# Kernel optimization log

Hardware: AMD Instinct MI355X
Metric: run time of the kernel (lower is better)

## Reference

```python
import jax, jax.numpy as jnp
from jax import lax
import numpy as np

B, C, H, W = 4, 256, 64, 64
CQK = C // 8  # 32


def conv3x3(x, w, b):
    # x: [B,C_in,H,W], w: [C_out,C_in,3,3], b: [C_out]
    y = lax.conv_general_dilated(x, w, window_strides=(1, 1), padding='SAME',
                                 dimension_numbers=('NCHW', 'OIHW', 'NCHW'))
    return y + b[None, :, None, None]


def setup_inputs() -> dict:
    key = jax.random.key(0)
    ks = jax.random.split(key, 8)
    scale = 0.02
    return {
        'x': jax.random.normal(ks[0], (B, C, H, W), dtype=jnp.float32),
        'wq': jax.random.normal(ks[1], (CQK, C, 3, 3), dtype=jnp.float32) * scale,
        'bq': jax.random.normal(ks[2], (CQK,), dtype=jnp.float32) * scale,
        'wk': jax.random.normal(ks[3], (CQK, C, 3, 3), dtype=jnp.float32) * scale,
        'bk': jax.random.normal(ks[4], (CQK,), dtype=jnp.float32) * scale,
        'wv': jax.random.normal(ks[5], (C, C, 3, 3), dtype=jnp.float32) * scale,
        'bv': jax.random.normal(ks[6], (C,), dtype=jnp.float32) * scale,
        'gamma': jax.random.normal(ks[7], (1,), dtype=jnp.float32) * scale,
    }


def reference(x, wq, bq, wk, bk, wv, bv, gamma):
    b, c, h, w = x.shape
    n = h * w
    # Q: [B, N, C//8]  (permute(0,2,1) of the flattened conv output)
    q = conv3x3(x, wq, bq).reshape(b, -1, n).transpose(0, 2, 1)
    # K: [B, C//8, N]
    k = conv3x3(x, wk, bk).reshape(b, -1, n)
    # s: [B, N_q, N_k]
    s = jnp.einsum('bqd,bdk->bqk', q, k)
    # NOTE: original uses Softmax(dim=-2), i.e. over the QUERY axis
    attn_T = jax.nn.softmax(s, axis=-2)
    # V: [B, C, N]
    v = conv3x3(x, wv, bv).reshape(b, c, n)
    # o = bmm(V, attn_T): [B, C, N]
    o = jnp.einsum('bcq,bqk->bck', v, attn_T).reshape(b, c, h, w)
    return x + gamma * o
```

## Files before the change

### kernel.cpp

```cpp
#include <hip/hip_runtime.h>
#include <cstddef>

#define N_PIX 4096
#define HW 64
#define LOG2E 1.4426950408889634f
#define SHIFT2 28.8539008177793f

typedef __attribute__((ext_vector_type(8))) short bf16x8;
typedef __attribute__((ext_vector_type(4))) float f32x4;

static __device__ __forceinline__ unsigned short f2bf(float f) {
    union { float f; unsigned u; } v; v.f = f;
    unsigned r = v.u + 0x7fffu + ((v.u >> 16) & 1u);
    return (unsigned short)(r >> 16);
}
static __device__ __forceinline__ float bf2f(unsigned short s) {
    union { unsigned u; float f; } v; v.u = (unsigned)s << 16;
    return v.f;
}
static __device__ __forceinline__ unsigned pack_bf16_trunc(float lo, float hi) {
    union { float f; unsigned u; } a, b; a.f = hi; b.f = lo;
    return __builtin_amdgcn_perm(a.u, b.u, 0x07060302u);
}

__global__ __launch_bounds__(256) void x_transpose(
    const float* __restrict__ x, unsigned short* __restrict__ xbf)
{
    __shared__ unsigned short Ts[64][72];
    const int tid = threadIdx.x;
    const int px0 = blockIdx.x * 64, ci0 = blockIdx.y * 64, b = blockIdx.z;
    const float* xb = x + ((size_t)b * 256 + ci0) * N_PIX;

#pragma unroll
    for (int r = 0; r < 4; ++r) {
        int c = r * 16 + (tid >> 4);
        int p4 = (tid & 15) * 4;
        float4 v = *(const float4*)&xb[(size_t)c * N_PIX + px0 + p4];
        Ts[c][p4 + 0] = f2bf(v.x);
        Ts[c][p4 + 1] = f2bf(v.y);
        Ts[c][p4 + 2] = f2bf(v.z);
        Ts[c][p4 + 3] = f2bf(v.w);
    }
    __syncthreads();
#pragma unroll
    for (int r = 0; r < 2; ++r) {
        int id = tid * 2 + r;
        int p = id >> 3, c8 = (id & 7) * 8;
        ushort4 lo, hi;
        lo.x = Ts[c8 + 0][p]; lo.y = Ts[c8 + 1][p];
        lo.z = Ts[c8 + 2][p]; lo.w = Ts[c8 + 3][p];
        hi.x = Ts[c8 + 4][p]; hi.y = Ts[c8 + 5][p];
        hi.z = Ts[c8 + 6][p]; hi.w = Ts[c8 + 7][p];
        size_t off = ((size_t)b * N_PIX + px0 + p) * 256 + ci0 + c8;
        *(ushort4*)&xbf[off]     = lo;
        *(ushort4*)&xbf[off + 4] = hi;
    }
}

__global__ __launch_bounds__(256) void w_transform(
    const float* __restrict__ wq, const float* __restrict__ wk,
    const float* __restrict__ wv, unsigned short* __restrict__ wAll)
{
    int gid = blockIdx.x * 256 + threadIdx.x;
    if (gid >= 72 * 320 * 4) return;
    int part = gid & 3;
    int m = (gid >> 2) % 320;
    int kb = gid / 1280;
    int t = kb >> 3;
    int ci0 = (kb & 7) * 32 + part * 8;
    const float* src; int co; float sc = 1.f;
    if (m < 256)      { src = wv; co = m; }
    else if (m < 288) { src = wq; co = m - 256; sc = LOG2E; }
    else              { src = wk; co = m - 288; }
    ushort4 lo, hi;
    lo.x = f2bf(sc * src[((size_t)co * 256 + ci0 + 0) * 9 + t]);
    lo.y = f2bf(sc * src[((size_t)co * 256 + ci0 + 1) * 9 + t]);
    lo.z = f2bf(sc * src[((size_t)co * 256 + ci0 + 2) * 9 + t]);
    lo.w = f2bf(sc * src[((size_t)co * 256 + ci0 + 3) * 9 + t]);
    hi.x = f2bf(sc * src[((size_t)co * 256 + ci0 + 4) * 9 + t]);
    hi.y = f2bf(sc * src[((size_t)co * 256 + ci0 + 5) * 9 + t]);
    hi.z = f2bf(sc * src[((size_t)co * 256 + ci0 + 6) * 9 + t]);
    hi.w = f2bf(sc * src[((size_t)co * 256 + ci0 + 7) * 9 + t]);
    size_t off = ((size_t)kb * 320 + m) * 32 + part * 8;
    *(ushort4*)&wAll[off]     = lo;
    *(ushort4*)&wAll[off + 4] = hi;
}

__global__ __launch_bounds__(256) void conv_gemm_v2(
    const unsigned short* __restrict__ xbf, const unsigned short* __restrict__ wAll,
    const float* __restrict__ bq, const float* __restrict__ bk,
    const float* __restrict__ bv,
    unsigned short* __restrict__ vbf, unsigned short* __restrict__ qt,
    unsigned short* __restrict__ kt)
{
    const int tid = threadIdx.x;
    const int w = tid >> 6, lane = tid & 63, quad = lane >> 4, l15 = lane & 15;
    const int px0 = blockIdx.x * 128;
    const int mt  = blockIdx.y;
    const int b   = blockIdx.z;
    const bool qk = (mt == 2);
    const int row0 = qk ? 256 : mt * 128;
    const int NCB  = qk ? 2 : 4;
    const int wc0  = (w & 1) * (qk ? 32 : 64);
    const int wp0  = (w >> 1) * 64;

    __shared__ unsigned short Bl[2][128 * 40];

    const unsigned short* xb = xbf + (size_t)b * N_PIX * 256;

    const int brow = tid >> 1;
    const int bp0  = (tid & 1) * 2;
    const int bswz = (brow >> 2) & 3;
    const int py = (px0 + brow) >> 6, pxc = brow & 63;

    f32x4 acc[4][4];
#pragma unroll
    for (int cb = 0; cb < 4; ++cb)
#pragma unroll
        for (int jb = 0; jb < 4; ++jb) acc[cb][jb] = (f32x4){0.f, 0.f, 0.f, 0.f};

    const unsigned short* aBase = wAll + ((size_t)(row0 + wc0 + l15) * 32 + quad * 8);

    auto load_a = [&](int kb, bf16x8* af) {
        const unsigned short* p = aBase + (size_t)kb * (320 * 32);
#pragma unroll
        for (int cb = 0; cb < 4; ++cb)
            if (cb < NCB) af[cb] = *(const bf16x8*)&p[cb * 512];
    };

    bf16x8 bS[2];
    auto load_b = [&](int kb) {
        int t = kb >> 3, ci0 = (kb & 7) << 5;
        int dy = t / 3 - 1, dx = t - (t / 3) * 3 - 1;
        int gy = py + dy, gx = pxc + dx;
        if ((unsigned)gy < 64u && (unsigned)gx < 64u) {
            const unsigned short* s = xb + ((size_t)(gy * 64 + gx) * 256 + ci0 + bp0 * 8);
            bS[0] = *(const bf16x8*)&s[0];
            bS[1] = *(const bf16x8*)&s[8];
        } else {
            bS[0] = (bf16x8){0,0,0,0,0,0,0,0};
            bS[1] = (bf16x8){0,0,0,0,0,0,0,0};
        }
    };
    auto store_b = [&](int buf) {
        int p0 = (bp0 + bswz) & 3;
        int p1 = (bp0 + 1 + bswz) & 3;
        *(bf16x8*)&Bl[buf][brow * 40 + p0 * 8] = bS[0];
        *(bf16x8*)&Bl[buf][brow * 40 + p1 * 8] = bS[1];
    };

    bf16x8 afC[4], afN[4];
    load_a(0, afC);
    load_b(0);
    store_b(0);

    for (int kb = 0; kb < 72; ++kb) {
        __syncthreads();
        const bool hasN = (kb + 1 < 72);
        if (hasN) { load_b(kb + 1); load_a(kb + 1, afN); }

        bf16x8 bf[4];
#pragma unroll
        for (int jb = 0; jb < 4; ++jb) {
            int row = wp0 + jb * 16 + l15;
            int pp = (quad + (row >> 2)) & 3;
            bf[jb] = *(const bf16x8*)&Bl[kb & 1][row * 40 + pp * 8];
        }
#pragma unroll
        for (int cb = 0; cb < 4; ++cb)
            if (cb < NCB)
#pragma unroll
                for (int jb = 0; jb < 4; ++jb)
                    acc[cb][jb] = __builtin_amdgcn_mfma_f32_16x16x32_bf16(
                        afC[cb], bf[jb], acc[cb][jb], 0, 0, 0);

        if (hasN) {
            store_b((kb + 1) & 1);
#pragma unroll
            for (int cb = 0; cb < 4; ++cb) afC[cb] = afN[cb];
        }
    }

    if (!qk) {
#pragma unroll
        for (int cb = 0; cb < 4; ++cb) {
            int c = mt * 128 + wc0 + cb * 16 + quad * 4;
#pragma unroll
            for (int r = 0; r < 4; ++r) {
                float bias = bv[c + r];
#pragma unroll
                for (int jb = 0; jb < 4; ++jb) {
                    int px = px0 + wp0 + jb * 16 + l15;
                    vbf[((size_t)b * 256 + c + r) * N_PIX + px] = f2bf(acc[cb][jb][r] + bias);
                }
            }
        }
    } else {
#pragma unroll
        for (int cb = 0; cb < 2; ++cb) {
            int cl = wc0 + cb * 16 + quad * 4;
#pragma unroll
            for (int r = 0; r < 4; ++r) {
                int c = cl + r;
                float bias = (c < 32) ? bq[c] * LOG2E : bk[c - 32];
#pragma unroll
                for (int jb = 0; jb < 4; ++jb) {
                    int px = px0 + wp0 + jb * 16 + l15;
                    unsigned short val = f2bf(acc[cb][jb][r] + bias);
                    if (c < 32)
                        qt[((size_t)b * N_PIX + px) * 32 + c] = val;
                    else
                        kt[((size_t)b * N_PIX + px) * 32 + (c - 32)] = val;
                }
            }
        }
    }
}

__global__ __launch_bounds__(256, 2) void fused_attn_mfma(
    const unsigned short* __restrict__ qt, const unsigned short* __restrict__ kt,
    const unsigned short* __restrict__ vbf,
    unsigned short* __restrict__ Abuf, float* __restrict__ lbuf, int iRange)
{
    const int tid  = threadIdx.x;
    const int w    = tid >> 6;
    const int lane = tid & 63;
    const int quad = lane >> 4;
    const int l15  = lane & 15;
    const int j0   = blockIdx.x * 128;
    const int b    = blockIdx.y;
    const int sp   = blockIdx.z;
    const int iBeg = sp * iRange;
    const int NI   = iRange / 64;

    const unsigned short* qtb = qt + (size_t)b * N_PIX * 32;
    const unsigned short* ktb = kt + (size_t)b * N_PIX * 32;
    const unsigned short* vb  = vbf + (size_t)b * 256 * N_PIX;

    __shared__ unsigned Pfrag[2][4096];
    __shared__ float lred[4][128];

    bf16x8 kf[8];
#pragma unroll
    for (int jb = 0; jb < 8; ++jb)
        kf[jb] = *(const bf16x8*)&ktb[((size_t)(j0 + jb * 16 + l15)) * 32 + quad * 8];

    f32x4 acc[4][8];
#pragma unroll
    for (int cb = 0; cb < 4; ++cb)
#pragma unroll
        for (int jb = 0; jb < 8; ++jb)
            acc[cb][jb] = (f32x4){0.f, 0.f, 0.f, 0.f};

    float lpart[8] = {0.f, 0.f, 0.f, 0.f, 0.f, 0.f, 0.f, 0.f};

    const int wFrag = w >> 1;
    const int wL    = ((w & 1) << 5) + ((quad >> 1) << 4) + l15;
    const int wEl2  = (quad & 1) << 1;

    bf16x8 va[2][4];

    auto s_phase = [&](bf16x8 qa, int buf) {
#pragma unroll
        for (int jb = 0; jb < 8; ++jb) {
            f32x4 s = __builtin_amdgcn_mfma_f32_16x16x32_bf16(
                qa, kf[jb], (f32x4){-SHIFT2, -SHIFT2, -SHIFT2, -SHIFT2}, 0, 0, 0);
            float p0 = __builtin_amdgcn_exp2f(s[0]);
            float p1 = __builtin_amdgcn_exp2f(s[1]);
            float p2 = __builtin_amdgcn_exp2f(s[2]);
            float p3 = __builtin_amdgcn_exp2f(s[3]);
            lpart[jb] += (p0 + p1) + (p2 + p3);
            unsigned u0 = pack_bf16_trunc(p0, p1);
            unsigned u1 = pack_bf16_trunc(p2, p3);
            unsigned base = (((jb << 1) + wFrag) * 64 + wL) * 4 + wEl2;
            Pfrag[buf][base]     = u0;
            Pfrag[buf][base + 1] = u1;
        }
    };

    auto load_qa = [&](int i0) {
        return *(const bf16x8*)&qtb[((size_t)(i0 + w * 16 + l15)) * 32 + quad * 8];
    };
    auto load_va = [&](int i0) {
#pragma unroll
        for (int ks = 0; ks < 2; ++ks)
#pragma unroll
            for (int cb = 0; cb < 4; ++cb)
                va[ks][cb] = *(const bf16x8*)&vb[((size_t)(w * 64 + cb * 16 + l15)) * N_PIX
                                                 + i0 + ks * 32 + quad * 8];
    };

    load_va(iBeg);
    s_phase(load_qa(iBeg), 0);

    for (int n = 0; n < NI; ++n) {
        __syncthreads();
        const bool hasN = (n + 1 < NI);
        const int inext = iBeg + (n + 1) * 64;
        bf16x8 qaN;
        if (hasN) qaN = load_qa(inext);

#pragma unroll
        for (int ks = 0; ks < 2; ++ks) {
            bf16x8 pb[8];
#pragma unroll
            for (int jb = 0; jb < 8; ++jb)
                pb[jb] = *(const bf16x8*)&Pfrag[n & 1][(((jb << 1) + ks) * 64 + lane) * 4];
#pragma unroll
            for (int cb = 0; cb < 4; ++cb)
#pragma unroll
                for (int jb = 0; jb < 8; ++jb)
                    acc[cb][jb] = __builtin_amdgcn_mfma_f32_16x16x32_bf16(
                        va[ks][cb], pb[jb], acc[cb][jb], 0, 0, 0);
        }

        if (hasN) {
            load_va(inext);
            s_phase(qaN, (n + 1) & 1);
        }
    }

#pragma unroll
    for (int jb = 0; jb < 8; ++jb) {
        float v = lpart[jb];
        v += __shfl_xor(v, 16, 64);
        v += __shfl_xor(v, 32, 64);
        lpart[jb] = v;
    }
    if (lane < 16) {
#pragma unroll
        for (int jb = 0; jb < 8; ++jb)
            lred[w][jb * 16 + l15] = lpart[jb];
    }
    __syncthreads();
    if (tid < 128) {
        float s = lred[0][tid] + lred[1][tid] + lred[2][tid] + lred[3][tid];
        lbuf[((size_t)sp * 4 + b) * N_PIX + j0 + tid] = s;
    }

    unsigned short* Ab = Abuf + ((size_t)sp * 4 + b) * 256 * N_PIX;
#pragma unroll
    for (int cb = 0; cb < 4; ++cb) {
        int c = w * 64 + cb * 16 + quad * 4;
#pragma unroll
        for (int jb = 0; jb < 8; ++jb) {
            int j = j0 + jb * 16 + l15;
#pragma unroll
            for (int r = 0; r < 4; ++r)
                Ab[(size_t)(c + r) * N_PIX + j] = f2bf(acc[cb][jb][r]);
        }
    }
}

__global__ __launch_bounds__(256) void combine_kernel(
    const unsigned short* __restrict__ A, const float* __restrict__ L,
    const float* __restrict__ x, const float* __restrict__ gamma,
    float* __restrict__ out, int split)
{
    const size_t CH = (size_t)4 * 256 * N_PIX;
    size_t flat = ((size_t)blockIdx.x * 256 + threadIdx.x) * 8;
    int j = (int)(flat & (N_PIX - 1));
    int b = (int)(flat >> 20);

    float a[8] = {0.f, 0.f, 0.f, 0.f, 0.f, 0.f, 0.f, 0.f};
    float l[8] = {0.f, 0.f, 0.f, 0.f, 0.f, 0.f, 0.f, 0.f};
    for (int s = 0; s < split; ++s) {
        ushort4 av0 = *(const ushort4*)&A[flat + (size_t)s * CH];
        ushort4 av1 = *(const ushort4*)&A[flat + (size_t)s * CH + 4];
        a[0] += bf2f(av0.x); a[1] += bf2f(av0.y); a[2] += bf2f(av0.z); a[3] += bf2f(av0.w);
        a[4] += bf2f(av1.x); a[5] += bf2f(av1.y); a[6] += bf2f(av1.z); a[7] += bf2f(av1.w);
        float4 l0 = *(const float4*)&L[((size_t)s * 4 + b) * N_PIX + j];
        float4 l1 = *(const float4*)&L[((size_t)s * 4 + b) * N_PIX + j + 4];
        l[0] += l0.x; l[1] += l0.y; l[2] += l0.z; l[3] += l0.w;
        l[4] += l1.x; l[5] += l1.y; l[6] += l1.z; l[7] += l1.w;
    }
    float g = gamma[0];
    float4 x0 = *(const float4*)&x[flat];
    float4 x1 = *(const float4*)&x[flat + 4];
    float4 o0, o1;
    o0.x = x0.x + g * a[0] / l[0];
    o0.y = x0.y + g * a[1] / l[1];
    o0.z = x0.z + g * a[2] / l[2];
    o0.w = x0.w + g * a[3] / l[3];
    o1.x = x1.x + g * a[4] / l[4];
    o1.y = x1.y + g * a[5] / l[5];
    o1.z = x1.z + g * a[6] / l[6];
    o1.w = x1.w + g * a[7] / l[7];
    *(float4*)&out[flat]     = o0;
    *(float4*)&out[flat + 4] = o1;
}

extern "C" void kernel_launch(void* const* d_in, const int* in_sizes, int n_in,
                              void* d_out, int out_size, void* d_ws, size_t ws_size,
                              hipStream_t stream)
{
    const float* x     = (const float*)d_in[0];
    const float* wq    = (const float*)d_in[1];
    const float* bq    = (const float*)d_in[2];
    const float* wk    = (const float*)d_in[3];
    const float* bk    = (const float*)d_in[4];
    const float* wv    = (const float*)d_in[5];
    const float* bv    = (const float*)d_in[6];
    const float* gamma = (const float*)d_in[7];
    float* out = (float*)d_out;

    const size_t szQTel  = (size_t)4 * N_PIX * 32;
    const size_t szVBFel = (size_t)4 * 256 * N_PIX;
    const size_t szXBFel = (size_t)4 * N_PIX * 256;
    const size_t szWel   = (size_t)72 * 320 * 32;
    const size_t fixedB  = (2 * szQTel + szVBFel + szXBFel + szWel) * 2;

    int split = 4;
    while (split > 1) {
        size_t need = fixedB
                    + (size_t)split * 4 * 256 * N_PIX * 2
                    + (size_t)split * 4 * N_PIX * 4;
        if (need <= ws_size) break;
        split >>= 1;
    }

    unsigned short* Abuf = (unsigned short*)d_ws;
    float* lbuf = (float*)(Abuf + (size_t)split * 4 * 256 * N_PIX);
    unsigned short* qt   = (unsigned short*)(lbuf + (size_t)split * 4 * N_PIX);
    unsigned short* kt   = qt + szQTel;
    unsigned short* vbf  = kt + szQTel;
    unsigned short* xbf  = vbf + szVBFel;
    unsigned short* wAll = xbf + szXBFel;

    x_transpose<<<dim3(N_PIX / 64, 4, 4), 256, 0, stream>>>(x, xbf);
    w_transform<<<dim3((72 * 320 * 4 + 255) / 256), 256, 0, stream>>>(wq, wk, wv, wAll);

    conv_gemm_v2<<<dim3(N_PIX / 128, 3, 4), 256, 0, stream>>>(
        xbf, wAll, bq, bk, bv, vbf, qt, kt);

    fused_attn_mfma<<<dim3(N_PIX / 128, 4, split), 256, 0, stream>>>(
        qt, kt, vbf, Abuf, lbuf, N_PIX / split);

    combine_kernel<<<dim3((4 * 256 * N_PIX) / (256 * 8)), 256, 0, stream>>>(
        Abuf, lbuf, x, gamma, out, split);
}
```

Baseline: 187.8 us.

## Halve conv GEMM pixel tile, double K step, raise occupancy target

The conv implicit-GEMM kernel now handles 64 pixels (one image row) per block instead of 128, and processes a K-chunk of 64 channels per stage using two MFMA sub-steps. It uses a 64-wide LDS row with an XOR-style swizzle and ping-pong A-fragment registers to avoid copies, plus launch_bounds(256,3). The aim is more blocks, for better CU fill and occupancy, and half as many barriers per block. The cost is less weight reuse per block and more redundant A loads across blocks.

```diff
diff --git a/kernel.cpp b/kernel.cpp
--- a/kernel.cpp
+++ b/kernel.cpp
@@ -86,7 +86,7 @@
     *(ushort4*)&wAll[off + 4] = hi;
 }
 
-__global__ __launch_bounds__(256) void conv_gemm_v2(
+__global__ __launch_bounds__(256, 3) void conv_gemm_v3(
     const unsigned short* __restrict__ xbf, const unsigned short* __restrict__ wAll,
     const float* __restrict__ bq, const float* __restrict__ bk,
     const float* __restrict__ bv,
@@ -95,46 +95,49 @@
 {
     const int tid = threadIdx.x;
     const int w = tid >> 6, lane = tid & 63, quad = lane >> 4, l15 = lane & 15;
-    const int px0 = blockIdx.x * 128;
+    const int bx  = blockIdx.x;
+    const int px0 = bx * 64;
     const int mt  = blockIdx.y;
     const int b   = blockIdx.z;
     const bool qk = (mt == 2);
     const int row0 = qk ? 256 : mt * 128;
     const int NCB  = qk ? 2 : 4;
     const int wc0  = (w & 1) * (qk ? 32 : 64);
-    const int wp0  = (w >> 1) * 64;
-
-    __shared__ unsigned short Bl[2][128 * 40];
+    const int wp0  = (w >> 1) * 32;
+
+    __shared__ unsigned short Bl[2][64 * 64];
 
     const unsigned short* xb = xbf + (size_t)b * N_PIX * 256;
 
-    const int brow = tid >> 1;
-    const int bp0  = (tid & 1) * 2;
-    const int bswz = (brow >> 2) & 3;
-    const int py = (px0 + brow) >> 6, pxc = brow & 63;
-
-    f32x4 acc[4][4];
+    const int brow = tid >> 2;
+    const int bp0  = (tid & 3) * 2;
+
+    f32x4 acc[4][2];
 #pragma unroll
     for (int cb = 0; cb < 4; ++cb)
 #pragma unroll
-        for (int jb = 0; jb < 4; ++jb) acc[cb][jb] = (f32x4){0.f, 0.f, 0.f, 0.f};
+        for (int jb = 0; jb < 2; ++jb) acc[cb][jb] = (f32x4){0.f, 0.f, 0.f, 0.f};
 
     const unsigned short* aBase = wAll + ((size_t)(row0 + wc0 + l15) * 32 + quad * 8);
 
-    auto load_a = [&](int kb, bf16x8* af) {
-        const unsigned short* p = aBase + (size_t)kb * (320 * 32);
-#pragma unroll
-        for (int cb = 0; cb < 4; ++cb)
-            if (cb < NCB) af[cb] = *(const bf16x8*)&p[cb * 512];
+    auto load_a = [&](int n, bf16x8 (&af)[2][4]) {
+        const unsigned short* p = aBase + (size_t)(2 * n) * (320 * 32);
+#pragma unroll
+        for (int kl = 0; kl < 2; ++kl)
+#pragma unroll
+            for (int cb = 0; cb < 4; ++cb)
+                if (cb < NCB) af[kl][cb] = *(const bf16x8*)&p[kl * (320 * 32) + cb * 512];
     };
 
     bf16x8 bS[2];
-    auto load_b = [&](int kb) {
-        int t = kb >> 3, ci0 = (kb & 7) << 5;
-        int dy = t / 3 - 1, dx = t - (t / 3) * 3 - 1;
-        int gy = py + dy, gx = pxc + dx;
+    auto load_b = [&](int n) {
+        int t  = n >> 2;
+        int ty = t / 3;
+        int dy = ty - 1, dx = t - ty * 3 - 1;
+        int gy = bx + dy, gx = brow + dx;
+        int cio = (n & 3) * 64 + (tid & 3) * 16;
         if ((unsigned)gy < 64u && (unsigned)gx < 64u) {
-            const unsigned short* s = xb + ((size_t)(gy * 64 + gx) * 256 + ci0 + bp0 * 8);
+            const unsigned short* s = xb + ((size_t)(gy * 64 + gx) * 256 + cio);
             bS[0] = *(const bf16x8*)&s[0];
             bS[1] = *(const bf16x8*)&s[8];
         } else {
@@ -143,42 +146,47 @@
         }
     };
     auto store_b = [&](int buf) {
-        int p0 = (bp0 + bswz) & 3;
-        int p1 = (bp0 + 1 + bswz) & 3;
-        *(bf16x8*)&Bl[buf][brow * 40 + p0 * 8] = bS[0];
-        *(bf16x8*)&Bl[buf][brow * 40 + p1 * 8] = bS[1];
-    };
-
-    bf16x8 afC[4], afN[4];
-    load_a(0, afC);
+        int p0 = (bp0 + brow) & 7;
+        int p1 = (bp0 + 1 + brow) & 7;
+        *(bf16x8*)&Bl[buf][brow * 64 + p0 * 8] = bS[0];
+        *(bf16x8*)&Bl[buf][brow * 64 + p1 * 8] = bS[1];
+    };
+
+    auto step = [&](int n, bf16x8 (&cur)[2][4], bf16x8 (&nxt)[2][4]) {
+        __syncthreads();
+        const bool hasN = (n + 1 < 36);
+        if (hasN) { load_b(n + 1); load_a(n + 1, nxt); }
+
+        bf16x8 bf[2][2];
+#pragma unroll
+        for (int kl = 0; kl < 2; ++kl)
+#pragma unroll
+            for (int jb = 0; jb < 2; ++jb) {
+                int row  = wp0 + jb * 16 + l15;
+                int part = kl * 4 + quad;
+                bf[kl][jb] = *(const bf16x8*)&Bl[n & 1][row * 64 + (((part + row) & 7) << 3)];
+            }
+#pragma unroll
+        for (int kl = 0; kl < 2; ++kl)
+#pragma unroll
+            for (int cb = 0; cb < 4; ++cb)
+                if (cb < NCB)
+#pragma unroll
+                    for (int jb = 0; jb < 2; ++jb)
+                        acc[cb][jb] = __builtin_amdgcn_mfma_f32_16x16x32_bf16(
+                            cur[kl][cb], bf[kl][jb], acc[cb][jb], 0, 0, 0);
+
+        if (hasN) store_b((n + 1) & 1);
+    };
+
+    bf16x8 afA[2][4], afB[2][4];
+    load_a(0, afA);
     load_b(0);
     store_b(0);
 
-    for (int kb = 0; kb < 72; ++kb) {
-        __syncthreads();
-        const bool hasN = (kb + 1 < 72);
-        if (hasN) { load_b(kb + 1); load_a(kb + 1, afN); }
-
-        bf16x8 bf[4];
-#pragma unroll
-        for (int jb = 0; jb < 4; ++jb) {
-            int row = wp0 + jb * 16 + l15;
-            int pp = (quad + (row >> 2)) & 3;
-            bf[jb] = *(const bf16x8*)&Bl[kb & 1][row * 40 + pp * 8];
-        }
-#pragma unroll
-        for (int cb = 0; cb < 4; ++cb)
-            if (cb < NCB)
-#pragma unroll
-                for (int jb = 0; jb < 4; ++jb)
-                    acc[cb][jb] = __builtin_amdgcn_mfma_f32_16x16x32_bf16(
-                        afC[cb], bf[jb], acc[cb][jb], 0, 0, 0);
-
-        if (hasN) {
-            store_b((kb + 1) & 1);
-#pragma unroll
-            for (int cb = 0; cb < 4; ++cb) afC[cb] = afN[cb];
-        }
+    for (int n = 0; n < 36; n += 2) {
+        step(n,     afA, afB);
+        step(n + 1, afB, afA);
     }
 
     if (!qk) {
@@ -189,7 +197,7 @@
             for (int r = 0; r < 4; ++r) {
                 float bias = bv[c + r];
 #pragma unroll
-                for (int jb = 0; jb < 4; ++jb) {
+                for (int jb = 0; jb < 2; ++jb) {
                     int px = px0 + wp0 + jb * 16 + l15;
                     vbf[((size_t)b * 256 + c + r) * N_PIX + px] = f2bf(acc[cb][jb][r] + bias);
                 }
@@ -204,7 +212,7 @@
                 int c = cl + r;
                 float bias = (c < 32) ? bq[c] * LOG2E : bk[c - 32];
 #pragma unroll
-                for (int jb = 0; jb < 4; ++jb) {
+                for (int jb = 0; jb < 2; ++jb) {
                     int px = px0 + wp0 + jb * 16 + l15;
                     unsigned short val = f2bf(acc[cb][jb][r] + bias);
                     if (c < 32)
@@ -430,7 +438,7 @@
     x_transpose<<<dim3(N_PIX / 64, 4, 4), 256, 0, stream>>>(x, xbf);
     w_transform<<<dim3((72 * 320 * 4 + 255) / 256), 256, 0, stream>>>(wq, wk, wv, wAll);
 
-    conv_gemm_v2<<<dim3(N_PIX / 128, 3, 4), 256, 0, stream>>>(
+    conv_gemm_v3<<<dim3(N_PIX / 64, 3, 4), 256, 0, stream>>>(
         xbf, wAll, bq, bk, bv, vbf, qt, kt);
 
     fused_attn_mfma<<<dim3(N_PIX / 128, 4, split), 256, 0, stream>>>(
```

Result: no change. 188.4 us (+0.3%).
